# Kernel tuning notes

Hardware: AMD Instinct MI355X
Metric: run time of the kernel (lower is better)

## Reference

```python
import jax, jax.numpy as jnp
import numpy as np
import math

DMODEL = 1024
N_EXPERTS = 32
EXPERT_SIZE = 512
N_HEADS = 4
TOKENS = 4096


def setup_inputs() -> dict:
    key = jax.random.key(0)
    k1, k2, k3, k4 = jax.random.split(key, 4)
    x = jax.random.normal(k1, (TOKENS, DMODEL), dtype=jnp.float32)
    keys_w = jax.random.normal(k2, (N_EXPERTS, DMODEL, EXPERT_SIZE), dtype=jnp.float32) * (DMODEL ** -0.5)
    values_w = jax.random.normal(k3, (N_EXPERTS, EXPERT_SIZE, DMODEL), dtype=jnp.float32) * ((N_EXPERTS * EXPERT_SIZE) ** -0.5)
    es = jax.random.normal(k4, (N_EXPERTS, DMODEL), dtype=jnp.float32) * (DMODEL ** -0.5)
    # renorm_keep_std(expert_sel, dim=1): row-normalize, then rescale to original global std
    std0 = jnp.std(es)
    es_n = es / jnp.linalg.norm(es, axis=1, keepdims=True)
    expert_sel = es_n * (std0 / jnp.std(es_n))
    return {"x": x, "keys": keys_w, "values": values_w, "expert_sel": expert_sel, "n_heads": N_HEADS}


def reference(x, keys, values, expert_sel, n_heads):
    # x: [T, d]; keys: [E, d, h]; values: [E, h, d]; expert_sel: [E, d]
    T, d = x.shape
    E = keys.shape[0]

    # routing logits
    sel_raw = x @ expert_sel.T  # [T, E]

    # entropy regularizer: mean (in log space) over tokens of log-softmax, then negative entropy
    logp = jax.nn.log_softmax(sel_raw, axis=-1)                 # [T, E]
    lm = jax.scipy.special.logsumexp(logp, axis=0) - math.log(T)  # [E]
    reg_loss = jnp.sum(lm * jnp.exp(lm))                        # -entropy_l(lm)

    # sigmoid selection + top-k experts per token
    sel = jax.nn.sigmoid(sel_raw)
    sel_val, sel_idx = jax.lax.top_k(sel, n_heads)              # [T, H]

    # expert up-projection (grouped GEMM): compute dense then gather selected experts
    scores_all = jnp.einsum('td,edh->teh', x, keys)             # [T, E, h]
    scores = jnp.take_along_axis(scores_all, sel_idx[:, :, None], axis=1)  # [T, H, h]
    scores = jax.nn.relu(scores) * sel_val[..., None]

    # combine: scatter weighted scores back to expert slots, then down-project
    onehot = jax.nn.one_hot(sel_idx, E, dtype=x.dtype)          # [T, H, E]
    dispatched = jnp.einsum('the,ths->tes', onehot, scores)     # [T, E, h]
    out = jnp.einsum('tes,esd->td', dispatched, values)         # [T, d]
    return out, reg_loss
```

## Files before the change

kernel.cpp:

```cpp
#include <hip/hip_runtime.h>
#include <hip/hip_bf16.h>

typedef unsigned short u16;
typedef unsigned int u32;
typedef __attribute__((ext_vector_type(4))) float f32x4;
typedef __attribute__((ext_vector_type(8))) short bf16x8;

#define TOKENS 4096
#define DMODEL 1024
#define NEXP 32
#define ESIZE 512

__device__ __forceinline__ u16 f2b(float f) {
  union { float f; u32 u; } v; v.f = f;
  u32 u = v.u;
  return (u16)((u + 0x7fffu + ((u >> 16) & 1u)) >> 16);
}

__device__ __forceinline__ u32 pk2(float a, float b) {
  union { __hip_bfloat162 h; u32 u; } v;
  v.h = __float22bfloat162_rn(make_float2(a, b));
  return v.u;
}

__device__ __forceinline__ float blo(u32 w) { union { u32 u; float f; } v; v.u = w << 16; return v.f; }
__device__ __forceinline__ float bhi(u32 w) { union { u32 u; float f; } v; v.u = w & 0xffff0000u; return v.f; }

typedef __attribute__((address_space(1))) const void as1_void;
typedef __attribute__((address_space(3))) void as3_void;
__device__ __forceinline__ void gl16(const void* g, void* l) {
  __builtin_amdgcn_global_load_lds((as1_void*)g, (as3_void*)l, 16, 0, 0);
}

__device__ __forceinline__ int swz(int row, int kk) {
  return row * 72 + ((((kk >> 3) ^ (row >> 2)) & 7) << 3) + (kk & 7);
}

__global__ __launch_bounds__(256) void k_esT(const float* __restrict__ es,
                                             float* __restrict__ esT4)
{
  int tid = threadIdx.x;
  int dblk = (blockIdx.x << 3) + (tid >> 5);
  int e = tid & 31;
  float4 v = *(const float4*)(es + (size_t)e * DMODEL + (dblk << 2));
  *((float4*)esT4 + (size_t)dblk * 32 + e) = v;
}

__global__ __launch_bounds__(256) void k_route(
    const float* __restrict__ x, const float* __restrict__ esT4,
    float* __restrict__ selval, u32* __restrict__ selpk,
    float* __restrict__ blockpart, u16* __restrict__ xb)
{
  __shared__ float part[4][8][32];
  __shared__ float ps[8][32];
  int tid = threadIdx.x;
  int w = tid >> 6, lane = tid & 63;
  int e = lane & 31, h = lane >> 5;
  int t0 = blockIdx.x << 3;

  const float4* ev = (const float4*)esT4 + (size_t)((w << 6) + (h << 5)) * 32 + e;
  const float4* xv = (const float4*)x + ((size_t)t0 << 8) + (w << 6) + (h << 5);

  float acc[8];
#pragma unroll
  for (int tk = 0; tk < 8; ++tk) acc[tk] = 0.f;

#pragma unroll 2
  for (int i = 0; i < 32; ++i) {
    float4 b = ev[(size_t)i * 32];
#pragma unroll
    for (int tk = 0; tk < 8; ++tk) {
      float4 a = xv[(tk << 8) + i];
      acc[tk] += a.x * b.x + a.y * b.y + a.z * b.z + a.w * b.w;
    }
  }
#pragma unroll
  for (int tk = 0; tk < 8; ++tk) {
    float s = acc[tk] + __shfl_xor(acc[tk], 32);
    if (h == 0) part[w][tk][e] = s;
  }
  __syncthreads();

  int tk = tid >> 5, ge = tid & 31;
  {
    float r = part[0][tk][ge] + part[1][tk][ge] + part[2][tk][ge] + part[3][tk][ge];
    int t = t0 + tk;

    float m = r;
#pragma unroll
    for (int mk = 16; mk; mk >>= 1) m = fmaxf(m, __shfl_xor(m, mk));
    float sx = __expf(r - m);
#pragma unroll
    for (int mk = 16; mk; mk >>= 1) sx += __shfl_xor(sx, mk);
    ps[tk][ge] = __expf(r - (m + __logf(sx)));

    u32 packed = 0;
    float v = r;
#pragma unroll
    for (int it = 0; it < 4; ++it) {
      float bv = v; int bi = ge;
#pragma unroll
      for (int mk = 16; mk; mk >>= 1) {
        float ov = __shfl_xor(bv, mk); int oi = __shfl_xor(bi, mk);
        if (ov > bv || (ov == bv && oi < bi)) { bv = ov; bi = oi; }
      }
      packed |= (u32)bi << (8 * it);
      if (ge == it) selval[t * 4 + it] = 1.f / (1.f + __expf(-bv));
      if (ge == bi) v = -3.0e38f;
    }
    if (ge == 0) selpk[t] = packed;
  }
  __syncthreads();
  if (tid < 32) {
    float s = 0.f;
#pragma unroll
    for (int j = 0; j < 8; ++j) s += ps[j][tid];
    blockpart[blockIdx.x * 32 + tid] = s;
  }

  if (xb) {
    const float4* src = (const float4*)x + ((size_t)blockIdx.x << 11);
    u16* dst = xb + ((size_t)blockIdx.x << 13);
#pragma unroll
    for (int j = 0; j < 8; ++j) {
      int idx = (j << 8) + tid;
      float4 a = src[idx];
      *(uint2*)(dst + (idx << 2)) = make_uint2(pk2(a.x, a.y), pk2(a.z, a.w));
    }
  }
}

__global__ __launch_bounds__(1024) void k_count(
    const u32* __restrict__ selpk, int* __restrict__ cnt, int* __restrict__ bucket)
{
  __shared__ int cl[32];
  int tid = threadIdx.x;
  if (tid < 32) cl[tid] = 0;
  __syncthreads();
  int ex[16], pos[16];
#pragma unroll
  for (int j = 0; j < 4; ++j) {
    int t = tid + (j << 10);
    u32 pk = selpk[t];
#pragma unroll
    for (int h = 0; h < 4; ++h) {
      int e = (pk >> (8 * h)) & 0xff;
      ex[j * 4 + h] = e;
      pos[j * 4 + h] = atomicAdd(&cl[e], 1);
    }
  }
#pragma unroll
  for (int j = 0; j < 4; ++j) {
    int t = tid + (j << 10);
#pragma unroll
    for (int h = 0; h < 4; ++h)
      bucket[ex[j * 4 + h] * TOKENS + pos[j * 4 + h]] = (t << 2) | h;
  }
  __syncthreads();
  if (tid < 32) cnt[tid] = cl[tid];
}

__global__ __launch_bounds__(256) void k_fin(const float* __restrict__ blockpart,
                                             float* __restrict__ out_reg)
{
  __shared__ float part[8][32];
  int tid = threadIdx.x;
  int e = tid & 31, c = tid >> 5;
  float s = 0.f;
  for (int b = c; b < 512; b += 8) s += blockpart[b * 32 + e];
  part[c][e] = s;
  __syncthreads();
  if (tid < 32) {
    float S = 0.f;
#pragma unroll
    for (int i = 0; i < 8; ++i) S += part[i][tid];
    float Pm = S * (1.0f / TOKENS);
    float rp = __logf(Pm) * Pm;
#pragma unroll
    for (int mk = 16; mk; mk >>= 1) rp += __shfl_xor(rp, mk);
    if (tid == 0) *out_reg = rp;
  }
}

__global__ __launch_bounds__(256) void k_tr(const float* __restrict__ src,
                                            u16* __restrict__ dst, int R, int C)
{
  __shared__ float tile[64][68];
  int e = blockIdx.z;
  int r0 = blockIdx.y << 6, c0 = blockIdx.x << 6;
  int t = threadIdx.x;
  int rr = t >> 2, cb = (t & 3) << 4;
  const float* sp = src + ((size_t)e * R + r0 + rr) * C + c0 + cb;
#pragma unroll
  for (int j = 0; j < 4; ++j)
    *(float4*)&tile[rr][cb + (j << 2)] = *(const float4*)(sp + (j << 2));
  __syncthreads();
  int wr = t >> 2, wb = (t & 3) << 4;
  u32 q[8];
#pragma unroll
  for (int j = 0; j < 8; ++j)
    q[j] = pk2(tile[wb + (j << 1)][wr], tile[wb + (j << 1) + 1][wr]);
  u16* dp = dst + ((size_t)e * C + c0 + wr) * R + r0 + wb;
  *(uint4*)dp = make_uint4(q[0], q[1], q[2], q[3]);
  *(uint4*)(dp + 8) = make_uint4(q[4], q[5], q[6], q[7]);
}

#define GEMM_MACROS                                                                          \
  int wm = (w >> 1) << 6, wn = (w & 1) << 6;                                                 \
  int w32 = w << 5;                                                                          \
  int lg16 = (((l & 7) ^ (l >> 3)) << 4);

#define STAGE(BUF, K0) do {                                                                  \
  _Pragma("unroll") for (int i_ = 0; i_ < 4; ++i_)                                           \
    gl16(gA[i_] + ((K0) << 1), (void*)&Ab[BUF][(((w << 2) + i_) << 9)]);                     \
  _Pragma("unroll") for (int i_ = 0; i_ < 4; ++i_)                                           \
    gl16(gB[i_] + ((K0) << 1), (void*)&Bb[BUF][(((w << 2) + i_) << 9)]);                     \
} while (0)

#define COMPUTE(CUR) do {                                                                    \
  _Pragma("unroll") for (int kh_ = 0; kh_ < 2; ++kh_) {                                      \
    bf16x8 af_[4], bf_[4];                                                                   \
    int gg_ = (kh_ << 2) + (l >> 4);                                                         \
    _Pragma("unroll") for (int mi_ = 0; mi_ < 4; ++mi_) {                                    \
      int row_ = wm + (mi_ << 4) + (l & 15);                                                 \
      af_[mi_] = *(const bf16x8*)&Ab[CUR][(row_ << 6) + ((gg_ ^ (row_ & 7)) << 3)];          \
    }                                                                                        \
    _Pragma("unroll") for (int ni_ = 0; ni_ < 4; ++ni_) {                                    \
      int row_ = wn + (ni_ << 4) + (l & 15);                                                 \
      bf_[ni_] = *(const bf16x8*)&Bb[CUR][(row_ << 6) + ((gg_ ^ (row_ & 7)) << 3)];          \
    }                                                                                        \
    _Pragma("unroll") for (int mi_ = 0; mi_ < 4; ++mi_)                                      \
      _Pragma("unroll") for (int ni_ = 0; ni_ < 4; ++ni_)                                    \
        acc[mi_][ni_] = __builtin_amdgcn_mfma_f32_16x16x32_bf16(af_[mi_], bf_[ni_],          \
                                                                acc[mi_][ni_], 0, 0, 0);     \
  }                                                                                          \
} while (0)

#define KLOOP(NT) do {                                                                       \
  STAGE(0, 0);                                                                               \
  STAGE(1, 64);                                                                              \
  _Pragma("unroll 1")                                                                        \
  for (int t_ = 0; t_ < (NT); ++t_) {                                                        \
    int cur_ = t_ & 1;                                                                       \
    if (t_ + 1 < (NT)) { asm volatile("s_waitcnt vmcnt(8)" ::: "memory"); }                  \
    else               { asm volatile("s_waitcnt vmcnt(0)" ::: "memory"); }                  \
    asm volatile("s_barrier" ::: "memory");                                                  \
    COMPUTE(cur_);                                                                           \
    asm volatile("s_barrier" ::: "memory");                                                  \
    if (t_ + 2 < (NT)) STAGE(cur_, (t_ + 2) << 6);                                           \
  }                                                                                          \
} while (0)

#define XCD_DECODE(SUB_NS_BITS)                                                              \
  int bid = blockIdx.x;                                                                      \
  int q_ = bid >> 3, sub_ = q_ & 15;                                                         \
  int e = ((q_ >> 4) << 3) | (bid & 7);                                                      \
  int ns = sub_ & ((1 << (SUB_NS_BITS)) - 1);                                                \
  int mz = sub_ >> (SUB_NS_BITS);

__global__ __launch_bounds__(256, 2) void k_up(
    const u16* __restrict__ xb, const u16* __restrict__ kb,
    const float* __restrict__ selval, const int* __restrict__ cnt,
    const int* __restrict__ bucket, const u16* __restrict__ zeros,
    u16* __restrict__ scores)
{
  XCD_DECODE(2);
  int ne = cnt[e];
  if ((mz << 7) >= ne) return;
  int nb0 = ns << 7;
  int tid = threadIdx.x, l = tid & 63, w = tid >> 6;

  __shared__ __align__(16) u16 Ab[2][8192];
  __shared__ __align__(16) u16 Bb[2][8192];
  __shared__ int slot_l[128];
  __shared__ float gate_l[128];

  GEMM_MACROS;

  const char* gB[4];
#pragma unroll
  for (int i = 0; i < 4; ++i) {
    int n = nb0 + w32 + (i << 3) + (l >> 3);
    gB[i] = (const char*)(kb + ((size_t)e * ESIZE + n) * DMODEL) + lg16;
  }

  for (int mt = mz; (mt << 7) < ne; mt += 4) {
    int row0 = mt << 7;
    int rem = ne - row0; if (rem > 128) rem = 128;
    __syncthreads();
    if (tid < 128) {
      int slot = -1; float g = 0.f;
      if (tid < rem) { slot = bucket[e * TOKENS + row0 + tid]; g = selval[slot]; }
      slot_l[tid] = slot; gate_l[tid] = g;
    }
    __syncthreads();

    const char* gA[4];
#pragma unroll
    for (int i = 0; i < 4; ++i) {
      int s = slot_l[w32 + (i << 3) + (l >> 3)];
      gA[i] = ((s >= 0) ? (const char*)(xb + (size_t)(s >> 2) * DMODEL)
                        : (const char*)zeros) + lg16;
    }

    f32x4 acc[4][4];
#pragma unroll
    for (int i = 0; i < 4; ++i)
#pragma unroll
      for (int j = 0; j < 4; ++j) acc[i][j] = (f32x4){0.f, 0.f, 0.f, 0.f};

    KLOOP(16);

#pragma unroll
    for (int mi = 0; mi < 4; ++mi) {
      int rbase = wm + (mi << 4) + ((l >> 4) << 2);
#pragma unroll
      for (int rr = 0; rr < 4; ++rr) {
        int r = rbase + rr;
        if (r < rem) {
          float g = gate_l[r];
          u16* so = scores + (size_t)slot_l[r] * ESIZE + nb0 + wn + (l & 15);
#pragma unroll
          for (int ni = 0; ni < 4; ++ni)
            so[ni << 4] = f2b(fmaxf(acc[mi][ni][rr], 0.f) * g);
        }
      }
    }
  }
}

__global__ __launch_bounds__(256, 2) void k_down(
    const u16* __restrict__ scores, const u16* __restrict__ vb,
    const int* __restrict__ cnt, const int* __restrict__ bucket,
    const u16* __restrict__ zeros, u16* __restrict__ stage)
{
  XCD_DECODE(3);
  int ne = cnt[e];
  if ((mz << 7) >= ne) return;
  int nb0 = ns << 7;
  int tid = threadIdx.x, l = tid & 63, w = tid >> 6;

  __shared__ __align__(16) u16 Ab[2][8192];
  __shared__ __align__(16) u16 Bb[2][8192];
  __shared__ int slot_l[128];

  GEMM_MACROS;

  const char* gB[4];
#pragma unroll
  for (int i = 0; i < 4; ++i) {
    int n = nb0 + w32 + (i << 3) + (l >> 3);
    gB[i] = (const char*)(vb + ((size_t)e * DMODEL + n) * ESIZE) + lg16;
  }

  for (int mt = mz; (mt << 7) < ne; mt += 2) {
    int row0 = mt << 7;
    int rem = ne - row0; if (rem > 128) rem = 128;
    __syncthreads();
    if (tid < 128) {
      int slot = -1;
      if (tid < rem) slot = bucket[e * TOKENS + row0 + tid];
      slot_l[tid] = slot;
    }
    __syncthreads();

    const char* gA[4];
#pragma unroll
    for (int i = 0; i < 4; ++i) {
      int s = slot_l[w32 + (i << 3) + (l >> 3)];
      gA[i] = ((s >= 0) ? (const char*)(scores + (size_t)s * ESIZE)
                        : (const char*)zeros) + lg16;
    }

    f32x4 acc[4][4];
#pragma unroll
    for (int i = 0; i < 4; ++i)
#pragma unroll
      for (int j = 0; j < 4; ++j) acc[i][j] = (f32x4){0.f, 0.f, 0.f, 0.f};

    KLOOP(8);

#pragma unroll
    for (int mi = 0; mi < 4; ++mi) {
      int rbase = wm + (mi << 4) + ((l >> 4) << 2);
#pragma unroll
      for (int rr = 0; rr < 4; ++rr) {
        int r = rbase + rr;
        if (r < rem) {
          u16* so = stage + (size_t)slot_l[r] * DMODEL + nb0 + wn + (l & 15);
#pragma unroll
          for (int ni = 0; ni < 4; ++ni)
            so[ni << 4] = f2b(acc[mi][ni][rr]);
        }
      }
    }
  }
}

__global__ __launch_bounds__(256) void k_final(const u16* __restrict__ stage,
                                               float* __restrict__ out)
{
  int tid = threadIdx.x;
  int t = (blockIdx.x << 1) + (tid >> 7);
  int d0 = (tid & 127) << 3;
  const u16* r0 = stage + ((size_t)t << 12) + d0;
  uint4 a0 = *(const uint4*)(r0);
  uint4 a1 = *(const uint4*)(r0 + 1024);
  uint4 a2 = *(const uint4*)(r0 + 2048);
  uint4 a3 = *(const uint4*)(r0 + 3072);
  float4 lo4, hi4;
  lo4.x = blo(a0.x) + blo(a1.x) + blo(a2.x) + blo(a3.x);
  lo4.y = bhi(a0.x) + bhi(a1.x) + bhi(a2.x) + bhi(a3.x);
  lo4.z = blo(a0.y) + blo(a1.y) + blo(a2.y) + blo(a3.y);
  lo4.w = bhi(a0.y) + bhi(a1.y) + bhi(a2.y) + bhi(a3.y);
  hi4.x = blo(a0.z) + blo(a1.z) + blo(a2.z) + blo(a3.z);
  hi4.y = bhi(a0.z) + bhi(a1.z) + bhi(a2.z) + bhi(a3.z);
  hi4.z = blo(a0.w) + blo(a1.w) + blo(a2.w) + blo(a3.w);
  hi4.w = bhi(a0.w) + bhi(a1.w) + bhi(a2.w) + bhi(a3.w);
  float* o = out + (size_t)t * DMODEL + d0;
  *(float4*)o = lo4;
  *(float4*)(o + 4) = hi4;
}

__global__ __launch_bounds__(256, 2) void k_up_rs(
    const float* __restrict__ x, const float* __restrict__ keys,
    const float* __restrict__ selval, const int* __restrict__ cnt,
    const int* __restrict__ bucket, u16* __restrict__ scores)
{
  int bid = blockIdx.x;
  int pair = bid & 127, mz = bid >> 7;
  int e = pair >> 2, ns = pair & 3;
  int ne = cnt[e];
  if ((mz << 7) >= ne) return;
  int nb0 = ns << 7;
  int tid = threadIdx.x;

  __shared__ __align__(16) u16 Abuf[2][128 * 72];
  __shared__ __align__(16) u16 Bbuf[2][128 * 72];
  __shared__ int slot_l[128];
  __shared__ float gate_l[128];

  const float* Kb = keys + (size_t)e * (DMODEL * ESIZE) + nb0;
  int arow = tid >> 1, ac0 = (tid & 1) << 5;
  int bn = tid & 31, bk0 = (tid >> 5) << 3;
  int lane = tid & 63, w = tid >> 6;
  int wm = (w >> 1) << 6, wn = (w & 1) << 6;

  for (int mt = mz; (mt << 7) < ne; mt += 4) {
    int row0 = mt << 7;
    int rem = ne - row0; if (rem > 128) rem = 128;
    __syncthreads();
    if (tid < 128) {
      int slot = -1; float g = 0.f;
      if (tid < rem) { slot = bucket[e * TOKENS + row0 + tid]; g = selval[slot]; }
      slot_l[tid] = slot; gate_l[tid] = g;
    }
    __syncthreads();

    int aslot = slot_l[arow];
    const float* xr = (aslot >= 0) ? (x + (size_t)(aslot >> 2) * DMODEL + ac0) : nullptr;
    const float* bp = Kb + (size_t)bk0 * ESIZE + (bn << 2);

    f32x4 acc[4][4];
#pragma unroll
    for (int i = 0; i < 4; ++i)
#pragma unroll
      for (int j = 0; j < 4; ++j) acc[i][j] = (f32x4){0.f, 0.f, 0.f, 0.f};

    float4 ar[8], br[8];
#define LOADA_UP(K) do { if (xr) { const float4* p_ = (const float4*)(xr + (K)); \
    _Pragma("unroll") for (int i_ = 0; i_ < 8; ++i_) ar[i_] = p_[i_]; } \
    else { _Pragma("unroll") for (int i_ = 0; i_ < 8; ++i_) ar[i_] = make_float4(0.f,0.f,0.f,0.f); } } while (0)
#define LOADB_RS(K, LDB) do { const float* q_ = bp + (size_t)(K) * (LDB); \
    _Pragma("unroll") for (int r_ = 0; r_ < 8; ++r_) br[r_] = *(const float4*)(q_ + (size_t)r_ * (LDB)); } while (0)
#define CVTWR_A(NB) do { _Pragma("unroll") for (int g_ = 0; g_ < 4; ++g_) { \
    u32 q0_ = pk2(ar[2*g_].x, ar[2*g_].y),   q1_ = pk2(ar[2*g_].z, ar[2*g_].w); \
    u32 q2_ = pk2(ar[2*g_+1].x, ar[2*g_+1].y), q3_ = pk2(ar[2*g_+1].z, ar[2*g_+1].w); \
    *(uint4*)&Abuf[NB][swz(arow, ac0 + 8*g_)] = make_uint4(q0_,q1_,q2_,q3_); } } while (0)
#define CVTWR_B(NB) do { \
    { u32 q0_=pk2(br[0].x,br[1].x),q1_=pk2(br[2].x,br[3].x),q2_=pk2(br[4].x,br[5].x),q3_=pk2(br[6].x,br[7].x); \
      *(uint4*)&Bbuf[NB][swz((bn<<2)+0, bk0)] = make_uint4(q0_,q1_,q2_,q3_); } \
    { u32 q0_=pk2(br[0].y,br[1].y),q1_=pk2(br[2].y,br[3].y),q2_=pk2(br[4].y,br[5].y),q3_=pk2(br[6].y,br[7].y); \
      *(uint4*)&Bbuf[NB][swz((bn<<2)+1, bk0)] = make_uint4(q0_,q1_,q2_,q3_); } \
    { u32 q0_=pk2(br[0].z,br[1].z),q1_=pk2(br[2].z,br[3].z),q2_=pk2(br[4].z,br[5].z),q3_=pk2(br[6].z,br[7].z); \
      *(uint4*)&Bbuf[NB][swz((bn<<2)+2, bk0)] = make_uint4(q0_,q1_,q2_,q3_); } \
    { u32 q0_=pk2(br[0].w,br[1].w),q1_=pk2(br[2].w,br[3].w),q2_=pk2(br[4].w,br[5].w),q3_=pk2(br[6].w,br[7].w); \
      *(uint4*)&Bbuf[NB][swz((bn<<2)+3, bk0)] = make_uint4(q0_,q1_,q2_,q3_); } } while (0)
#define MFMA_RS(CUR) do { _Pragma("unroll") for (int kh_ = 0; kh_ < 2; ++kh_) { \
    int kk_ = (kh_ << 5) | ((lane >> 4) << 3); \
    bf16x8 af_[4], bf_[4]; \
    _Pragma("unroll") for (int mi_ = 0; mi_ < 4; ++mi_) \
      af_[mi_] = *(const bf16x8*)&Abuf[CUR][swz(wm + (mi_ << 4) + (lane & 15), kk_)]; \
    _Pragma("unroll") for (int ni_ = 0; ni_ < 4; ++ni_) \
      bf_[ni_] = *(const bf16x8*)&Bbuf[CUR][swz(wn + (ni_ << 4) + (lane & 15), kk_)]; \
    _Pragma("unroll") for (int mi_ = 0; mi_ < 4; ++mi_) \
      _Pragma("unroll") for (int ni_ = 0; ni_ < 4; ++ni_) \
        acc[mi_][ni_] = __builtin_amdgcn_mfma_f32_16x16x32_bf16(af_[mi_], bf_[ni_], acc[mi_][ni_], 0, 0, 0); \
  } } while (0)

    LOADA_UP(0); LOADB_RS(0, ESIZE);
    CVTWR_A(0); CVTWR_B(0);
    __syncthreads();
    int cur = 0;
    for (int k0 = 0; k0 < DMODEL; k0 += 64) {
      bool late = (k0 + 64 >= DMODEL);
      if (!late) { LOADA_UP(k0 + 64); LOADB_RS(k0 + 64, ESIZE); }
      MFMA_RS(cur);
      if (!late) { CVTWR_A(cur ^ 1); CVTWR_B(cur ^ 1); }
      __syncthreads();
      cur ^= 1;
    }

#pragma unroll
    for (int mi = 0; mi < 4; ++mi) {
      int rbase = wm + (mi << 4) + ((lane >> 4) << 2);
#pragma unroll
      for (int rr = 0; rr < 4; ++rr) {
        int r = rbase + rr;
        if (r < rem) {
          float g = gate_l[r];
          u16* so = scores + (size_t)slot_l[r] * ESIZE + nb0 + wn + (lane & 15);
#pragma unroll
          for (int ni = 0; ni < 4; ++ni)
            so[ni << 4] = f2b(fmaxf(acc[mi][ni][rr], 0.f) * g);
        }
      }
    }
#undef LOADA_UP
#undef LOADB_RS
#undef CVTWR_A
#undef CVTWR_B
#undef MFMA_RS
  }
}

__global__ __launch_bounds__(256, 2) void k_down_rs(
    const u16* __restrict__ scores, const float* __restrict__ values,
    const int* __restrict__ cnt, const int* __restrict__ bucket,
    u16* __restrict__ stage, float* __restrict__ out)
{
  int bid = blockIdx.x;
  int pair = bid & 255, mz = bid >> 8;
  int e = pair >> 3, ns = pair & 7;
  int ne = cnt[e];
  if ((mz << 7) >= ne) return;
  int nb0 = ns << 7;
  int tid = threadIdx.x;

  __shared__ __align__(16) u16 Abuf[2][128 * 72];
  __shared__ __align__(16) u16 Bbuf[2][128 * 72];
  __shared__ int slot_l[128];

  const float* Vb = values + (size_t)e * (ESIZE * DMODEL) + nb0;
  int arow = tid >> 1, ac0 = (tid & 1) << 5;
  int bn = tid & 31, bk0 = (tid >> 5) << 3;
  int lane = tid & 63, w = tid >> 6;
  int wm = (w >> 1) << 6, wn = (w & 1) << 6;

  for (int mt = mz; (mt << 7) < ne; mt += 2) {
    int row0 = mt << 7;
    int rem = ne - row0; if (rem > 128) rem = 128;
    __syncthreads();
    if (tid < 128) {
      int slot = -1;
      if (tid < rem) slot = bucket[e * TOKENS + row0 + tid];
      slot_l[tid] = slot;
    }
    __syncthreads();

    int aslot = slot_l[arow];
    const u16* sr = (aslot >= 0) ? (scores + (size_t)aslot * ESIZE + ac0) : nullptr;
    const float* bp = Vb + (size_t)bk0 * DMODEL + (bn << 2);

    f32x4 acc[4][4];
#pragma unroll
    for (int i = 0; i < 4; ++i)
#pragma unroll
      for (int j = 0; j < 4; ++j) acc[i][j] = (f32x4){0.f, 0.f, 0.f, 0.f};

    uint4 a4[4]; float4 br[8];
#define LOADA_DN(K) do { if (sr) { const uint4* p_ = (const uint4*)(sr + (K)); \
    _Pragma("unroll") for (int i_ = 0; i_ < 4; ++i_) a4[i_] = p_[i_]; } \
    else { _Pragma("unroll") for (int i_ = 0; i_ < 4; ++i_) a4[i_] = make_uint4(0,0,0,0); } } while (0)
#define LOADB_RS(K, LDB) do { const float* q_ = bp + (size_t)(K) * (LDB); \
    _Pragma("unroll") for (int r_ = 0; r_ < 8; ++r_) br[r_] = *(const float4*)(q_ + (size_t)r_ * (LDB)); } while (0)
#define WR_A(NB) do { _Pragma("unroll") for (int g_ = 0; g_ < 4; ++g_) \
    *(uint4*)&Abuf[NB][swz(arow, ac0 + 8*g_)] = a4[g_]; } while (0)
#define CVTWR_B(NB) do { \
    { u32 q0_=pk2(br[0].x,br[1].x),q1_=pk2(br[2].x,br[3].x),q2_=pk2(br[4].x,br[5].x),q3_=pk2(br[6].x,br[7].x); \
      *(uint4*)&Bbuf[NB][swz((bn<<2)+0, bk0)] = make_uint4(q0_,q1_,q2_,q3_); } \
    { u32 q0_=pk2(br[0].y,br[1].y),q1_=pk2(br[2].y,br[3].y),q2_=pk2(br[4].y,br[5].y),q3_=pk2(br[6].y,br[7].y); \
      *(uint4*)&Bbuf[NB][swz((bn<<2)+1, bk0)] = make_uint4(q0_,q1_,q2_,q3_); } \
    { u32 q0_=pk2(br[0].z,br[1].z),q1_=pk2(br[2].z,br[3].z),q2_=pk2(br[4].z,br[5].z),q3_=pk2(br[6].z,br[7].z); \
      *(uint4*)&Bbuf[NB][swz((bn<<2)+2, bk0)] = make_uint4(q0_,q1_,q2_,q3_); } \
    { u32 q0_=pk2(br[0].w,br[1].w),q1_=pk2(br[2].w,br[3].w),q2_=pk2(br[4].w,br[5].w),q3_=pk2(br[6].w,br[7].w); \
      *(uint4*)&Bbuf[NB][swz((bn<<2)+3, bk0)] = make_uint4(q0_,q1_,q2_,q3_); } } while (0)
#define MFMA_RS(CUR) do { _Pragma("unroll") for (int kh_ = 0; kh_ < 2; ++kh_) { \
    int kk_ = (kh_ << 5) | ((lane >> 4) << 3); \
    bf16x8 af_[4], bf_[4]; \
    _Pragma("unroll") for (int mi_ = 0; mi_ < 4; ++mi_) \
      af_[mi_] = *(const bf16x8*)&Abuf[CUR][swz(wm + (mi_ << 4) + (lane & 15), kk_)]; \
    _Pragma("unroll") for (int ni_ = 0; ni_ < 4; ++ni_) \
      bf_[ni_] = *(const bf16x8*)&Bbuf[CUR][swz(wn + (ni_ << 4) + (lane & 15), kk_)]; \
    _Pragma("unroll") for (int mi_ = 0; mi_ < 4; ++mi_) \
      _Pragma("unroll") for (int ni_ = 0; ni_ < 4; ++ni_) \
        acc[mi_][ni_] = __builtin_amdgcn_mfma_f32_16x16x32_bf16(af_[mi_], bf_[ni_], acc[mi_][ni_], 0, 0, 0); \
  } } while (0)

    LOADA_DN(0); LOADB_RS(0, DMODEL);
    WR_A(0); CVTWR_B(0);
    __syncthreads();
    int cur = 0;
    for (int k0 = 0; k0 < ESIZE; k0 += 64) {
      bool late = (k0 + 64 >= ESIZE);
      if (!late) { LOADA_DN(k0 + 64); LOADB_RS(k0 + 64, DMODEL); }
      MFMA_RS(cur);
      if (!late) { WR_A(cur ^ 1); CVTWR_B(cur ^ 1); }
      __syncthreads();
      cur ^= 1;
    }

#pragma unroll
    for (int mi = 0; mi < 4; ++mi) {
      int rbase = wm + (mi << 4) + ((lane >> 4) << 2);
#pragma unroll
      for (int rr = 0; rr < 4; ++rr) {
        int r = rbase + rr;
        if (r < rem) {
          if (stage) {
            u16* so = stage + (size_t)slot_l[r] * DMODEL + nb0 + wn + (lane & 15);
#pragma unroll
            for (int ni = 0; ni < 4; ++ni)
              so[ni << 4] = f2b(acc[mi][ni][rr]);
          } else {
            int t = slot_l[r] >> 2;
            float* oo = out + (size_t)t * DMODEL + nb0 + wn + (lane & 15);
#pragma unroll
            for (int ni = 0; ni < 4; ++ni)
              atomicAdd(&oo[ni << 4], acc[mi][ni][rr]);
          }
        }
      }
    }
#undef LOADA_DN
#undef LOADB_RS
#undef WR_A
#undef CVTWR_B
#undef MFMA_RS
  }
}

extern "C" void kernel_launch(void* const* d_in, const int* in_sizes, int n_in,
                              void* d_out, int out_size, void* d_ws, size_t ws_size,
                              hipStream_t stream) {
  (void)in_sizes; (void)n_in;
  const float* x      = (const float*)d_in[0];
  const float* keys   = (const float*)d_in[1];
  const float* values = (const float*)d_in[2];
  const float* es     = (const float*)d_in[3];
  float* out = (float*)d_out;

  char* W = (char*)d_ws;
  int*   cnt       = (int*)W;
  u16*   zeros     = (u16*)(W + 4 * 1024);
  u32*   selpk     = (u32*)(W + 16 * 1024);
  float* selval    = (float*)(W + 64 * 1024);
  float* blockpart = (float*)(W + 128 * 1024);
  int*   bucket    = (int*)(W + 512 * 1024);
  float* esT4      = (float*)(W + 1280 * 1024);

  bool big = ws_size >= (90ull << 20);
  u16* xb = big ? (u16*)(W + 2ull * 1024 * 1024) : nullptr;

  k_esT<<<32, 256, 0, stream>>>(es, esT4);
  k_route<<<TOKENS / 8, 256, 0, stream>>>(x, esT4, selval, selpk, blockpart, xb);
  k_count<<<1, 1024, 0, stream>>>(selpk, cnt, bucket);
  k_fin<<<1, 256, 0, stream>>>(blockpart, out + (size_t)out_size - 1);

  if (big) {
    u16* scores = (u16*)(W + 10ull * 1024 * 1024);
    u16* kb     = (u16*)(W + 26ull * 1024 * 1024);
    u16* vb     = (u16*)(W + 58ull * 1024 * 1024);
    u16* stage  = kb;
    hipMemsetAsync(zeros, 0, 4096, stream);
    k_tr<<<dim3(ESIZE / 64, DMODEL / 64, NEXP), 256, 0, stream>>>(keys, kb, DMODEL, ESIZE);
    k_tr<<<dim3(DMODEL / 64, ESIZE / 64, NEXP), 256, 0, stream>>>(values, vb, ESIZE, DMODEL);
    k_up<<<512, 256, 0, stream>>>(xb, kb, selval, cnt, bucket, zeros, scores);
    k_down<<<512, 256, 0, stream>>>(scores, vb, cnt, bucket, zeros, stage);
    k_final<<<TOKENS / 2, 256, 0, stream>>>(stage, out);
  } else {
    u16* scores = (u16*)(W + 2ull * 1024 * 1024);
    bool big50 = ws_size >= (50ull << 20);
    u16* stage = big50 ? (u16*)(W + 18ull * 1024 * 1024) : nullptr;
    if (!big50)
      hipMemsetAsync(d_out, 0, (size_t)out_size * sizeof(float), stream);
    k_up_rs<<<512, 256, 0, stream>>>(x, keys, selval, cnt, bucket, scores);
    k_down_rs<<<512, 256, 0, stream>>>(scores, values, cnt, bucket, stage, out);
    if (big50)
      k_final<<<TOKENS / 2, 256, 0, stream>>>(stage, out);
  }
}
```

Baseline: 171.8 us.

## Fuse fp32 weight transpose and bf16 conversion into expert GEMM B-tile loads

Removes the separate k_tr transpose/convert kernels for keys and values. The up and down GEMMs now read fp32 weights straight from global memory into registers, pack them to bf16 and write them into a padded, swizzled LDS tile, with the next tile's loads issued before the current compute. This saves a full read and write pass over both weight tensors, but each GEMM block re-reads fp32 weights, which is twice the bytes of bf16. It also uses a full vmcnt/lgkmcnt drain and barrier per k-step instead of the earlier deeper async pipeline.

```diff
diff --git a/kernel.cpp b/kernel.cpp
--- a/kernel.cpp
+++ b/kernel.cpp
@@ -182,52 +182,45 @@
   }
 }
 
-__global__ __launch_bounds__(256) void k_tr(const float* __restrict__ src,
-                                            u16* __restrict__ dst, int R, int C)
-{
-  __shared__ float tile[64][68];
-  int e = blockIdx.z;
-  int r0 = blockIdx.y << 6, c0 = blockIdx.x << 6;
-  int t = threadIdx.x;
-  int rr = t >> 2, cb = (t & 3) << 4;
-  const float* sp = src + ((size_t)e * R + r0 + rr) * C + c0 + cb;
-#pragma unroll
-  for (int j = 0; j < 4; ++j)
-    *(float4*)&tile[rr][cb + (j << 2)] = *(const float4*)(sp + (j << 2));
-  __syncthreads();
-  int wr = t >> 2, wb = (t & 3) << 4;
-  u32 q[8];
-#pragma unroll
-  for (int j = 0; j < 8; ++j)
-    q[j] = pk2(tile[wb + (j << 1)][wr], tile[wb + (j << 1) + 1][wr]);
-  u16* dp = dst + ((size_t)e * C + c0 + wr) * R + r0 + wb;
-  *(uint4*)dp = make_uint4(q[0], q[1], q[2], q[3]);
-  *(uint4*)(dp + 8) = make_uint4(q[4], q[5], q[6], q[7]);
-}
-
 #define GEMM_MACROS                                                                          \
   int wm = (w >> 1) << 6, wn = (w & 1) << 6;                                                 \
   int w32 = w << 5;                                                                          \
-  int lg16 = (((l & 7) ^ (l >> 3)) << 4);
-
-#define STAGE(BUF, K0) do {                                                                  \
+  int lg16 = (((l & 7) ^ (l >> 3)) << 4);                                                    \
+  int bn = tid & 31, bk0 = (tid >> 5) << 3;
+
+#define STAGE_A(BUF, K0) do {                                                                \
   _Pragma("unroll") for (int i_ = 0; i_ < 4; ++i_)                                           \
     gl16(gA[i_] + ((K0) << 1), (void*)&Ab[BUF][(((w << 2) + i_) << 9)]);                     \
-  _Pragma("unroll") for (int i_ = 0; i_ < 4; ++i_)                                           \
-    gl16(gB[i_] + ((K0) << 1), (void*)&Bb[BUF][(((w << 2) + i_) << 9)]);                     \
 } while (0)
 
-#define COMPUTE(CUR) do {                                                                    \
+#define LOADB_F(K0, LDB) do {                                                                \
+  _Pragma("unroll") for (int r_ = 0; r_ < 8; ++r_)                                           \
+    br[r_] = *(const float4*)(bp + (size_t)((K0) + bk0 + r_) * (LDB));                       \
+} while (0)
+
+#define CVT_B(NB) do {                                                                       \
+  { int r_=(bn<<2);   *(uint4*)&Bb[NB][swz(r_,bk0)] = make_uint4(                            \
+      pk2(br[0].x,br[1].x),pk2(br[2].x,br[3].x),pk2(br[4].x,br[5].x),pk2(br[6].x,br[7].x)); }\
+  { int r_=(bn<<2)+1; *(uint4*)&Bb[NB][swz(r_,bk0)] = make_uint4(                            \
+      pk2(br[0].y,br[1].y),pk2(br[2].y,br[3].y),pk2(br[4].y,br[5].y),pk2(br[6].y,br[7].y)); }\
+  { int r_=(bn<<2)+2; *(uint4*)&Bb[NB][swz(r_,bk0)] = make_uint4(                            \
+      pk2(br[0].z,br[1].z),pk2(br[2].z,br[3].z),pk2(br[4].z,br[5].z),pk2(br[6].z,br[7].z)); }\
+  { int r_=(bn<<2)+3; *(uint4*)&Bb[NB][swz(r_,bk0)] = make_uint4(                            \
+      pk2(br[0].w,br[1].w),pk2(br[2].w,br[3].w),pk2(br[4].w,br[5].w),pk2(br[6].w,br[7].w)); }\
+} while (0)
+
+#define COMPUTE_MIX(CUR) do {                                                                \
   _Pragma("unroll") for (int kh_ = 0; kh_ < 2; ++kh_) {                                      \
     bf16x8 af_[4], bf_[4];                                                                   \
     int gg_ = (kh_ << 2) + (l >> 4);                                                         \
+    int kk_ = (kh_ << 5) | ((l >> 4) << 3);                                                  \
     _Pragma("unroll") for (int mi_ = 0; mi_ < 4; ++mi_) {                                    \
       int row_ = wm + (mi_ << 4) + (l & 15);                                                 \
       af_[mi_] = *(const bf16x8*)&Ab[CUR][(row_ << 6) + ((gg_ ^ (row_ & 7)) << 3)];          \
     }                                                                                        \
     _Pragma("unroll") for (int ni_ = 0; ni_ < 4; ++ni_) {                                    \
       int row_ = wn + (ni_ << 4) + (l & 15);                                                 \
-      bf_[ni_] = *(const bf16x8*)&Bb[CUR][(row_ << 6) + ((gg_ ^ (row_ & 7)) << 3)];          \
+      bf_[ni_] = *(const bf16x8*)&Bb[CUR][swz(row_, kk_)];                                   \
     }                                                                                        \
     _Pragma("unroll") for (int mi_ = 0; mi_ < 4; ++mi_)                                      \
       _Pragma("unroll") for (int ni_ = 0; ni_ < 4; ++ni_)                                    \
@@ -236,18 +229,23 @@
   }                                                                                          \
 } while (0)
 
-#define KLOOP(NT) do {                                                                       \
-  STAGE(0, 0);                                                                               \
-  STAGE(1, 64);                                                                              \
+#define DRAIN_BAR() do {                                                                     \
+  asm volatile("s_waitcnt vmcnt(0) lgkmcnt(0)" ::: "memory");                                \
+  asm volatile("s_barrier" ::: "memory");                                                    \
+} while (0)
+
+#define KLOOP_FUSED(NT, LDB) do {                                                            \
+  LOADB_F(0, LDB);                                                                           \
+  STAGE_A(0, 0);                                                                             \
+  CVT_B(0);                                                                                  \
+  DRAIN_BAR();                                                                               \
   _Pragma("unroll 1")                                                                        \
   for (int t_ = 0; t_ < (NT); ++t_) {                                                        \
     int cur_ = t_ & 1;                                                                       \
-    if (t_ + 1 < (NT)) { asm volatile("s_waitcnt vmcnt(8)" ::: "memory"); }                  \
-    else               { asm volatile("s_waitcnt vmcnt(0)" ::: "memory"); }                  \
-    asm volatile("s_barrier" ::: "memory");                                                  \
-    COMPUTE(cur_);                                                                           \
-    asm volatile("s_barrier" ::: "memory");                                                  \
-    if (t_ + 2 < (NT)) STAGE(cur_, (t_ + 2) << 6);                                           \
+    if (t_ + 1 < (NT)) { LOADB_F((t_ + 1) << 6, LDB); STAGE_A(cur_ ^ 1, (t_ + 1) << 6); }    \
+    COMPUTE_MIX(cur_);                                                                       \
+    if (t_ + 1 < (NT)) CVT_B(cur_ ^ 1);                                                      \
+    DRAIN_BAR();                                                                             \
   }                                                                                          \
 } while (0)
 
@@ -259,7 +257,7 @@
   int mz = sub_ >> (SUB_NS_BITS);
 
 __global__ __launch_bounds__(256, 2) void k_up(
-    const u16* __restrict__ xb, const u16* __restrict__ kb,
+    const u16* __restrict__ xb, const float* __restrict__ keys,
     const float* __restrict__ selval, const int* __restrict__ cnt,
     const int* __restrict__ bucket, const u16* __restrict__ zeros,
     u16* __restrict__ scores)
@@ -271,18 +269,13 @@
   int tid = threadIdx.x, l = tid & 63, w = tid >> 6;
 
   __shared__ __align__(16) u16 Ab[2][8192];
-  __shared__ __align__(16) u16 Bb[2][8192];
+  __shared__ __align__(16) u16 Bb[2][128 * 72];
   __shared__ int slot_l[128];
   __shared__ float gate_l[128];
 
   GEMM_MACROS;
 
-  const char* gB[4];
-#pragma unroll
-  for (int i = 0; i < 4; ++i) {
-    int n = nb0 + w32 + (i << 3) + (l >> 3);
-    gB[i] = (const char*)(kb + ((size_t)e * ESIZE + n) * DMODEL) + lg16;
-  }
+  const float* bp = keys + (size_t)e * (DMODEL * ESIZE) + nb0 + (bn << 2);
 
   for (int mt = mz; (mt << 7) < ne; mt += 4) {
     int row0 = mt << 7;
@@ -309,7 +302,8 @@
 #pragma unroll
       for (int j = 0; j < 4; ++j) acc[i][j] = (f32x4){0.f, 0.f, 0.f, 0.f};
 
-    KLOOP(16);
+    float4 br[8];
+    KLOOP_FUSED(16, ESIZE);
 
 #pragma unroll
     for (int mi = 0; mi < 4; ++mi) {
@@ -330,7 +324,7 @@
 }
 
 __global__ __launch_bounds__(256, 2) void k_down(
-    const u16* __restrict__ scores, const u16* __restrict__ vb,
+    const u16* __restrict__ scores, const float* __restrict__ values,
     const int* __restrict__ cnt, const int* __restrict__ bucket,
     const u16* __restrict__ zeros, u16* __restrict__ stage)
 {
@@ -341,17 +335,12 @@
   int tid = threadIdx.x, l = tid & 63, w = tid >> 6;
 
   __shared__ __align__(16) u16 Ab[2][8192];
-  __shared__ __align__(16) u16 Bb[2][8192];
+  __shared__ __align__(16) u16 Bb[2][128 * 72];
   __shared__ int slot_l[128];
 
   GEMM_MACROS;
 
-  const char* gB[4];
-#pragma unroll
-  for (int i = 0; i < 4; ++i) {
-    int n = nb0 + w32 + (i << 3) + (l >> 3);
-    gB[i] = (const char*)(vb + ((size_t)e * DMODEL + n) * ESIZE) + lg16;
-  }
+  const float* bp = values + (size_t)e * (ESIZE * DMODEL) + nb0 + (bn << 2);
 
   for (int mt = mz; (mt << 7) < ne; mt += 2) {
     int row0 = mt << 7;
@@ -378,7 +367,8 @@
 #pragma unroll
       for (int j = 0; j < 4; ++j) acc[i][j] = (f32x4){0.f, 0.f, 0.f, 0.f};
 
-    KLOOP(8);
+    float4 br[8];
+    KLOOP_FUSED(8, DMODEL);
 
 #pragma unroll
     for (int mi = 0; mi < 4; ++mi) {
@@ -669,7 +659,7 @@
   int*   bucket    = (int*)(W + 512 * 1024);
   float* esT4      = (float*)(W + 1280 * 1024);
 
-  bool big = ws_size >= (90ull << 20);
+  bool big = ws_size >= (60ull << 20);
   u16* xb = big ? (u16*)(W + 2ull * 1024 * 1024) : nullptr;
 
   k_esT<<<32, 256, 0, stream>>>(es, esT4);
@@ -679,14 +669,10 @@
 
   if (big) {
     u16* scores = (u16*)(W + 10ull * 1024 * 1024);
-    u16* kb     = (u16*)(W + 26ull * 1024 * 1024);
-    u16* vb     = (u16*)(W + 58ull * 1024 * 1024);
-    u16* stage  = kb;
+    u16* stage  = (u16*)(W + 26ull * 1024 * 1024);
     hipMemsetAsync(zeros, 0, 4096, stream);
-    k_tr<<<dim3(ESIZE / 64, DMODEL / 64, NEXP), 256, 0, stream>>>(keys, kb, DMODEL, ESIZE);
-    k_tr<<<dim3(DMODEL / 64, ESIZE / 64, NEXP), 256, 0, stream>>>(values, vb, ESIZE, DMODEL);
-    k_up<<<512, 256, 0, stream>>>(xb, kb, selval, cnt, bucket, zeros, scores);
-    k_down<<<512, 256, 0, stream>>>(scores, vb, cnt, bucket, zeros, stage);
+    k_up<<<512, 256, 0, stream>>>(xb, keys, selval, cnt, bucket, zeros, scores);
+    k_down<<<512, 256, 0, stream>>>(scores, values, cnt, bucket, zeros, stage);
     k_final<<<TOKENS / 2, 256, 0, stream>>>(stage, out);
   } else {
     u16* scores = (u16*)(W + 2ull * 1024 * 1024);
```

Result: slower. 188.0 us (+9.4%).
